# Optimization experiments

Hardware: AMD Instinct MI355X
Metric: run time of the kernel (lower is better)

Reference implementation:

```python
import jax, jax.numpy as jnp
import numpy as np

P_TOKENS = 200  # num_prompt_tokens
N_HEADS = 4


def setup_inputs() -> dict:
    key = jax.random.key(0)
    ks = jax.random.split(key, 6)
    B, N, C = 64, 1224, 1024
    D = 256  # bottleneck / down_size
    s = 0.02
    return {
        "x": jax.random.normal(ks[0], (B, N, C), dtype=jnp.float32),
        "down_W": jax.random.normal(ks[1], (D, C), dtype=jnp.float32) * s,
        "down_b": jnp.zeros((D,), jnp.float32),
        "up_W": jax.random.normal(ks[2], (C, D), dtype=jnp.float32) * s,
        "up_b": jnp.zeros((C,), jnp.float32),
        "in_proj_W": jax.random.normal(ks[3], (3 * D, D), dtype=jnp.float32) * s,
        "in_proj_b": jnp.zeros((3 * D,), jnp.float32),
        "out_proj_W": jax.random.normal(ks[4], (D, D), dtype=jnp.float32) * s,
        "out_proj_b": jnp.zeros((D,), jnp.float32),
        "gate": jnp.float32(1.0),
    }


def _forward(x, down_W, down_b, up_W, up_b, in_proj_W, in_proj_b,
             out_proj_W, out_proj_b, gate):
    B, N, C = x.shape
    E = down_W.shape[0]
    hd = E // N_HEADS
    # down projection + exact GELU (torch nn.GELU default)
    down = jax.nn.gelu(x @ down_W.T + down_b, approximate=False)  # [B,N,E]
    prompt = down[:, :P_TOKENS, :]   # [B,P,E]
    tok = down[:, P_TOKENS:, :]      # [B,T,E]
    # --- nn.MultiheadAttention(prompt, prompt, prompt) ---
    qkv = prompt @ in_proj_W.T + in_proj_b            # [B,P,3E]
    q, k, v = jnp.split(qkv, 3, axis=-1)
    def heads(t):
        return t.reshape(B, P_TOKENS, N_HEADS, hd)
    q, k, v = heads(q), heads(k), heads(v)
    attn = jnp.einsum('bqhd,bkhd->bhqk', q, k) / jnp.sqrt(jnp.float32(hd))
    attn = jax.nn.softmax(attn, axis=-1)
    sa = jnp.einsum('bhqk,bkhd->bqhd', attn, v).reshape(B, P_TOKENS, E)
    sa = sa @ out_proj_W.T + out_proj_b               # [B,P,E]
    # --- manual cross attention prompt -> tokens ---
    scale = jnp.float32(E) ** -0.5
    cross = jax.nn.softmax(jnp.einsum('bpe,bte->bpt', sa, tok) * scale, axis=-1)
    prompt_out = jnp.einsum('bpt,bte->bpe', cross, tok)  # [B,P,E]
    combined = jnp.concatenate([prompt_out, tok], axis=1)  # [B,N,E]
    up = combined @ up_W.T + up_b                          # [B,N,C]
    return gate * up


def reference(x, down_W, down_b, up_W, up_b, in_proj_W, in_proj_b,
              out_proj_W, out_proj_b, gate):
    return _forward(x, down_W, down_b, up_W, up_b, in_proj_W, in_proj_b,
                    out_proj_W, out_proj_b, gate)
```

## Files before the change

kernel.cpp:

```cpp
#include <hip/hip_runtime.h>
#include <math.h>

#define BB 64
#define NN 1224
#define CC 1024
#define DD 256
#define PP 200
#define TT 1024
#define HH 4
#define HDD 64

typedef __attribute__((ext_vector_type(8))) short bf16x8;
typedef __attribute__((ext_vector_type(4))) float f32x4;
typedef unsigned short u16;
typedef unsigned long long u64;

__device__ __forceinline__ u16 f2bf(float f) {
  union { float f; unsigned int u; } v; v.f = f;
  unsigned int r = v.u + 0x7FFF + ((v.u >> 16) & 1);
  return (u16)(r >> 16);
}
__device__ __forceinline__ float bf2f(u16 h) {
  union { unsigned int u; float f; } v; v.u = ((unsigned int)h) << 16;
  return v.f;
}
__device__ __forceinline__ unsigned int pk2(float a, float b) {
  return (unsigned int)f2bf(a) | ((unsigned int)f2bf(b) << 16);
}
__device__ __forceinline__ void gload16(const void* g, void* l) {
  __builtin_amdgcn_global_load_lds(
      (const __attribute__((address_space(1))) void*)g,
      (__attribute__((address_space(3))) void*)l, 16, 0, 0);
}
__device__ __forceinline__ f32x4 ntld4(const float* p) {
  return __builtin_nontemporal_load((const f32x4*)p);
}

static const size_t SZ_DOWN = (size_t)BB * NN * DD * 2;
static const size_t SZ_TOKT = (size_t)BB * DD * TT * 2;
static const size_t SZ_Q    = (size_t)BB * HH * PP * HDD * 2;
static const size_t SZ_SCORES = (size_t)BB * PP * TT * 2;

static const size_t B_DOWN   = 0;
static const size_t B_TOKT   = B_DOWN + SZ_DOWN;
static const size_t B_POOL   = B_TOKT + SZ_TOKT;
static const size_t B_QB     = B_POOL;
static const size_t B_KB     = B_QB + SZ_Q;
static const size_t B_VB     = B_KB + SZ_Q;
static const size_t B_SA     = B_VB + SZ_Q;
static const size_t B_SA2    = B_SA + SZ_Q;
static const size_t B_PBF    = B_POOL;
static const size_t B_POUTBF = B_SA2;
static const size_t B_SCORES = B_SA2 + SZ_Q;
static const size_t B_W      = B_SCORES + SZ_SCORES * 2;
static const size_t B_WD     = B_W;
static const size_t B_WU     = B_WD + 524288;
static const size_t B_WIP    = B_WU + 524288;
static const size_t B_WOP    = B_WIP + 393216;

#define MFMA_STEP64(Ab, Bb) \
  _Pragma("unroll") \
  for (int kk = 0; kk < 64; kk += 32) { \
    bf16x8 af[4], bfr[2]; \
    _Pragma("unroll") \
    for (int mi = 0; mi < 4; ++mi) { \
      const int R = mi * 16 + (lane & 15); \
      const int byt = (R * 128 + (kk + (lane >> 4) * 8) * 2) ^ ((R & 7) << 4); \
      af[mi] = *(const bf16x8*)((const char*)Ab + byt); \
    } \
    _Pragma("unroll") \
    for (int ni = 0; ni < 2; ++ni) { \
      const int R = wave * 32 + ni * 16 + (lane & 15); \
      const int byt = (R * 128 + (kk + (lane >> 4) * 8) * 2) ^ ((R & 7) << 4); \
      bfr[ni] = *(const bf16x8*)((const char*)Bb + byt); \
    } \
    _Pragma("unroll") \
    for (int mi = 0; mi < 4; ++mi) \
      _Pragma("unroll") \
      for (int ni = 0; ni < 2; ++ni) \
        acc[mi][ni] = __builtin_amdgcn_mfma_f32_16x16x32_bf16(af[mi], bfr[ni], acc[mi][ni], 0, 0, 0); \
  }

#define GLOAD_A1(Ab, SRC) \
  { \
    const int L = wave * 1024 + lane * 16; \
    const int r = L >> 7; \
    const int ce = ((L & 127) ^ ((r & 7) << 4)) >> 1; \
    gload16((SRC), (char*)Ab + wave * 1024); \
  }

#define GLOAD_B4(Bb, SRC) \
  _Pragma("unroll") \
  for (int ii = 0; ii < 4; ++ii) { \
    const int slot = wave * 4 + ii; \
    const int L = slot * 1024 + lane * 16; \
    const int r = L >> 7; \
    const int ce = ((L & 127) ^ ((r & 7) << 4)) >> 1; \
    gload16((SRC), (char*)Bb + slot * 1024); \
  }

#define PIPE_WAIT(N) asm volatile("s_waitcnt vmcnt(" #N ")" ::: "memory");
#define PIPE_BAR() \
  __builtin_amdgcn_s_barrier(); \
  __builtin_amdgcn_sched_barrier(0);
#define PIPE_END() \
  asm volatile("s_waitcnt lgkmcnt(0)" ::: "memory"); \
  __builtin_amdgcn_s_barrier(); \
  __builtin_amdgcn_sched_barrier(0);

__global__ __launch_bounds__(256) void k_castw(const float* __restrict__ dW,
                                               const float* __restrict__ uW,
                                               const float* __restrict__ iW,
                                               const float* __restrict__ oW,
                                               u16* __restrict__ dWb, u16* __restrict__ uWb,
                                               u16* __restrict__ iWb, u16* __restrict__ oWb)
{
  const int id = blockIdx.x * 256 + threadIdx.x;
  const float* s; u16* d; int off;
  if (id < 65536)       { s = dW; d = dWb; off = id; }
  else if (id < 131072) { s = uW; d = uWb; off = id - 65536; }
  else if (id < 180224) { s = iW; d = iWb; off = id - 131072; }
  else                  { s = oW; d = oWb; off = id - 180224; }
  const float4 v = ((const float4*)s)[off];
  uint2 p; p.x = pk2(v.x, v.y); p.y = pk2(v.z, v.w);
  *(uint2*)&d[(size_t)off * 4] = p;
}

__global__ __launch_bounds__(512) void k_down(const float* __restrict__ x,
                                              const u16* __restrict__ Wd,
                                              const float* __restrict__ bias,
                                              u16* __restrict__ out)
{
  __shared__ u16 Ab[2][64 * 64];
  __shared__ u16 Bb[2][256 * 64];
  const int tid = threadIdx.x;
  const int lane = tid & 63, wave = tid >> 6;
  f32x4 acc[4][2] = {};
  const int m0 = blockIdx.x * 64;
  const int ar0 = tid >> 4;
  const int c4 = (tid & 15) * 4;

  f32x4 areg[2];
#pragma unroll
  for (int i = 0; i < 2; ++i)
    areg[i] = ntld4(&x[(size_t)(m0 + ar0 + 32 * i) * CC + c4]);
#pragma unroll
  for (int i = 0; i < 2; ++i) {
    const int r = ar0 + 32 * i;
    uint2 p; p.x = pk2(areg[i].x, areg[i].y); p.y = pk2(areg[i].z, areg[i].w);
    *(uint2*)((char*)Ab[0] + ((r * 128 + c4 * 2) ^ ((r & 7) << 4))) = p;
  }
  GLOAD_B4(Bb[0], &Wd[(size_t)r * CC + 0 + ce])
#pragma unroll
  for (int i = 0; i < 2; ++i)
    areg[i] = ntld4(&x[(size_t)(m0 + ar0 + 32 * i) * CC + 64 + c4]);

  for (int it = 0; it < 16; ++it) {
    const int cur = it & 1;
    if (it < 14) {
#pragma unroll
      for (int i = 0; i < 2; ++i) {
        const int r = ar0 + 32 * i;
        uint2 p; p.x = pk2(areg[i].x, areg[i].y); p.y = pk2(areg[i].z, areg[i].w);
        *(uint2*)((char*)Ab[cur ^ 1] + ((r * 128 + c4 * 2) ^ ((r & 7) << 4))) = p;
      }
      const int kx = (it + 2) * 64;
#pragma unroll
      for (int i = 0; i < 2; ++i)
        areg[i] = ntld4(&x[(size_t)(m0 + ar0 + 32 * i) * CC + kx + c4]);
      const int kb = (it + 1) * 64;
      GLOAD_B4(Bb[cur ^ 1], &Wd[(size_t)r * CC + kb + ce])
      asm volatile("s_waitcnt vmcnt(6) lgkmcnt(0)" ::: "memory");
    } else if (it == 14) {
#pragma unroll
      for (int i = 0; i < 2; ++i) {
        const int r = ar0 + 32 * i;
        uint2 p; p.x = pk2(areg[i].x, areg[i].y); p.y = pk2(areg[i].z, areg[i].w);
        *(uint2*)((char*)Ab[cur ^ 1] + ((r * 128 + c4 * 2) ^ ((r & 7) << 4))) = p;
      }
      GLOAD_B4(Bb[cur ^ 1], &Wd[(size_t)r * CC + 960 + ce])
      asm volatile("s_waitcnt vmcnt(4) lgkmcnt(0)" ::: "memory");
    } else {
      asm volatile("s_waitcnt vmcnt(0) lgkmcnt(0)" ::: "memory");
    }
    PIPE_BAR()
    MFMA_STEP64(Ab[cur], Bb[cur])
    PIPE_END()
  }
#pragma unroll
  for (int mi = 0; mi < 4; ++mi) {
#pragma unroll
    for (int ni = 0; ni < 2; ++ni) {
      const int col = wave * 32 + ni * 16 + (lane & 15);
      const float bv = bias[col];
#pragma unroll
      for (int r = 0; r < 4; ++r) {
        const int row = m0 + mi * 16 + (lane >> 4) * 4 + r;
        float v = acc[mi][ni][r] + bv;
        v = 0.5f * v * (1.f + erff(v * 0.7071067811865475f));
        out[(size_t)row * DD + col] = f2bf(v);
      }
    }
  }
}

__global__ __launch_bounds__(256) void k_tokT(const u16* __restrict__ down,
                                              u16* __restrict__ tokT)
{
  __shared__ u16 Ls[64][68];
  const int b = blockIdx.z;
  const int t0 = blockIdx.x * 64, e0 = blockIdx.y * 64;
  const int tid = threadIdx.x;
#pragma unroll
  for (int it = 0; it < 4; ++it) {
    const int idx = tid + 256 * it;
    const int r = idx >> 4, c4 = (idx & 15) * 4;
    const u64 v = *(const u64*)&down[((size_t)(b * NN + PP + t0 + r)) * DD + e0 + c4];
    *(u64*)&Ls[r][c4] = v;
  }
  __syncthreads();
#pragma unroll
  for (int it = 0; it < 4; ++it) {
    const int idx = tid + 256 * it;
    const int re = idx >> 4, c4 = (idx & 15) * 4;
    u64 pk = (u64)Ls[c4 + 0][re] | ((u64)Ls[c4 + 1][re] << 16) |
             ((u64)Ls[c4 + 2][re] << 32) | ((u64)Ls[c4 + 3][re] << 48);
    *(u64*)&tokT[((size_t)(b * DD + e0 + re)) * TT + t0 + c4] = pk;
  }
}

__global__ __launch_bounds__(512) void k_qkv(const u16* __restrict__ down,
                                             const u16* __restrict__ Wip,
                                             const float* __restrict__ bias,
                                             u16* __restrict__ qb,
                                             u16* __restrict__ kb,
                                             u16* __restrict__ vb)
{
  __shared__ u16 Ab[2][64 * 64];
  __shared__ u16 Bb[2][256 * 64];
  const int tid = threadIdx.x;
  const int lane = tid & 63, wave = tid >> 6;
  f32x4 acc[4][2] = {};
  const int m0 = blockIdx.x * 64;
  const int nt = blockIdx.y;

#define QKV_A(BUF, K0) GLOAD_A1(BUF, ({ const int m = m0 + r; const int b = m / PP; const int p = m - b * PP; \
                    &down[((size_t)(b * NN + p)) * DD + (K0) + ce]; }))
  QKV_A(Ab[0], 0)
  GLOAD_B4(Bb[0], &Wip[(size_t)(nt * 256 + r) * DD + 0 + ce])
  for (int it = 0; it < 4; ++it) {
    const int cur = it & 1;
    if (it < 3) {
      const int k0 = (it + 1) * 64;
      QKV_A(Ab[cur ^ 1], k0)
      GLOAD_B4(Bb[cur ^ 1], &Wip[(size_t)(nt * 256 + r) * DD + k0 + ce])
      PIPE_WAIT(5)
    } else { PIPE_WAIT(0) }
    PIPE_BAR()
    MFMA_STEP64(Ab[cur], Bb[cur])
    PIPE_END()
  }
#undef QKV_A
  u16* dst = (nt == 0) ? qb : ((nt == 1) ? kb : vb);
#pragma unroll
  for (int mi = 0; mi < 4; ++mi) {
#pragma unroll
    for (int ni = 0; ni < 2; ++ni) {
      const int n = wave * 32 + ni * 16 + (lane & 15);
      const float bv = bias[nt * 256 + n];
      const int h = n >> 6, dd = n & 63;
#pragma unroll
      for (int r = 0; r < 4; ++r) {
        const int m = m0 + mi * 16 + (lane >> 4) * 4 + r;
        const int b = m / PP, p = m - b * PP;
        dst[(((size_t)(b * HH + h)) * PP + p) * HDD + dd] = f2bf(acc[mi][ni][r] + bv);
      }
    }
  }
}

__global__ __launch_bounds__(256) void k_attn(const u16* __restrict__ qb,
                                              const u16* __restrict__ kb,
                                              const u16* __restrict__ vb,
                                              u16* __restrict__ sa)
{
  __shared__ u16 Ks[208 * 64];
  __shared__ u16 Vt[64 * 232];
  __shared__ u16 Pb[4 * 16 * 232];
  const int tid = threadIdx.x, lane = tid & 63, wave = tid >> 6;
  const int bh = blockIdx.x;
  const size_t kvbase = (size_t)bh * (PP * HDD);

  for (int it = 0; it < 13; ++it) {
    const int idx = tid + 256 * it;
    if (idx < 3200) {
      const int e = idx * 4;
      const int j = e >> 6, d = e & 63;
      const u64 kv = *(const u64*)&kb[kvbase + e];
      const int byt = (j * 128 + d * 2) ^ ((j & 7) << 4);
      *(u64*)((char*)Ks + byt) = kv;
      const u64 vv = *(const u64*)&vb[kvbase + e];
      const u16* vp = (const u16*)&vv;
#pragma unroll
      for (int w = 0; w < 4; ++w) Vt[(d + w) * 232 + j] = vp[w];
    }
  }
  if (tid < 128) {
    const int rr = 200 + (tid >> 4), c = (tid & 15) * 4;
    const int byt = (rr * 128 + c * 2) ^ ((rr & 7) << 4);
    *(u64*)((char*)Ks + byt) = 0ULL;
  }
#pragma unroll
  for (int w = 0; w < 2; ++w) {
    const int idx = tid + 256 * w;
    const int d = idx >> 3, cg = idx & 7;
    *(u64*)&Vt[d * 232 + 200 + cg * 4] = 0ULL;
  }
  {
    u16* pw = Pb + wave * (16 * 232);
#pragma unroll
    for (int w = 0; w < 2; ++w) {
      const int idx = lane + 64 * w;
      if (idx < 96) {
        const int row = idx / 6, cg = idx - row * 6;
        *(u64*)&pw[row * 232 + 208 + cg * 4] = 0ULL;
      }
    }
  }
  __syncthreads();

  const int b_ = bh >> 2, h = bh & 3;
  const u16* qbase = qb + kvbase;
  u16* pw = Pb + wave * (16 * 232);

  for (int f = wave; f < 13; f += 4) {
    int qrow = f * 16 + (lane & 15); if (qrow > 199) qrow = 199;
    bf16x8 qa[2];
#pragma unroll
    for (int kk = 0; kk < 2; ++kk)
      qa[kk] = *(const bf16x8*)&qbase[(size_t)qrow * 64 + kk * 32 + (lane >> 4) * 8];

    f32x4 s[13];
#pragma unroll
    for (int nf = 0; nf < 13; ++nf) {
      const int R = nf * 16 + (lane & 15);
      f32x4 a = {};
#pragma unroll
      for (int kk = 0; kk < 2; ++kk) {
        const int byt = (R * 128 + (kk * 32 + (lane >> 4) * 8) * 2) ^ ((R & 7) << 4);
        const bf16x8 kf = *(const bf16x8*)((const char*)Ks + byt);
        a = __builtin_amdgcn_mfma_f32_16x16x32_bf16(qa[kk], kf, a, 0, 0, 0);
      }
      s[nf] = a;
    }
    float mx[4] = {-1e30f, -1e30f, -1e30f, -1e30f};
#pragma unroll
    for (int nf = 0; nf < 13; ++nf) {
      const int col = nf * 16 + (lane & 15);
#pragma unroll
      for (int r = 0; r < 4; ++r) {
        float v = (col < PP) ? s[nf][r] * 0.125f : -INFINITY;
        s[nf][r] = v;
        mx[r] = fmaxf(mx[r], v);
      }
    }
#pragma unroll
    for (int off = 1; off < 16; off <<= 1)
#pragma unroll
      for (int r = 0; r < 4; ++r) mx[r] = fmaxf(mx[r], __shfl_xor(mx[r], off));
    float sum[4] = {0.f, 0.f, 0.f, 0.f};
#pragma unroll
    for (int nf = 0; nf < 13; ++nf)
#pragma unroll
      for (int r = 0; r < 4; ++r) {
        const float e = expf(s[nf][r] - mx[r]);
        s[nf][r] = e;
        sum[r] += e;
      }
#pragma unroll
    for (int off = 1; off < 16; off <<= 1)
#pragma unroll
      for (int r = 0; r < 4; ++r) sum[r] += __shfl_xor(sum[r], off);
    float inv[4];
#pragma unroll
    for (int r = 0; r < 4; ++r) inv[r] = 1.f / sum[r];
#pragma unroll
    for (int nf = 0; nf < 13; ++nf) {
      const int col = nf * 16 + (lane & 15);
#pragma unroll
      for (int r = 0; r < 4; ++r) {
        const int row = (lane >> 4) * 4 + r;
        pw[row * 232 + col] = f2bf(s[nf][r] * inv[r]);
      }
    }
    f32x4 o[4] = {};
#pragma unroll
    for (int kk = 0; kk < 7; ++kk) {
      const bf16x8 pa = *(const bf16x8*)((const char*)pw +
                         ((lane & 15) * 232 + kk * 32 + (lane >> 4) * 8) * 2);
#pragma unroll
      for (int nf4 = 0; nf4 < 4; ++nf4) {
        const bf16x8 vv = *(const bf16x8*)((const char*)Vt +
                           (((lane & 15) + 16 * nf4) * 232 + kk * 32 + (lane >> 4) * 8) * 2);
        o[nf4] = __builtin_amdgcn_mfma_f32_16x16x32_bf16(pa, vv, o[nf4], 0, 0, 0);
      }
    }
#pragma unroll
    for (int nf4 = 0; nf4 < 4; ++nf4) {
      const int d = (lane & 15) + 16 * nf4;
#pragma unroll
      for (int r = 0; r < 4; ++r) {
        const int p = f * 16 + (lane >> 4) * 4 + r;
        if (p < PP)
          sa[((size_t)(b_ * PP + p)) * DD + h * HDD + d] = f2bf(o[nf4][r]);
      }
    }
  }
}

__global__ __launch_bounds__(512) void k_oproj(const u16* __restrict__ A,
                                               const u16* __restrict__ Wop,
                                               const float* __restrict__ bias,
                                               u16* __restrict__ out)
{
  __shared__ u16 Ab[2][64 * 64];
  __shared__ u16 Bb[2][256 * 64];
  const int tid = threadIdx.x;
  const int lane = tid & 63, wave = tid >> 6;
  f32x4 acc[4][2] = {};
  const int m0 = blockIdx.x * 64;

  GLOAD_A1(Ab[0], &A[(size_t)(m0 + r) * DD + 0 + ce])
  GLOAD_B4(Bb[0], &Wop[(size_t)r * DD + 0 + ce])
  for (int it = 0; it < 4; ++it) {
    const int cur = it & 1;
    if (it < 3) {
      const int k0 = (it + 1) * 64;
      GLOAD_A1(Ab[cur ^ 1], &A[(size_t)(m0 + r) * DD + k0 + ce])
      GLOAD_B4(Bb[cur ^ 1], &Wop[(size_t)r * DD + k0 + ce])
      PIPE_WAIT(5)
    } else { PIPE_WAIT(0) }
    PIPE_BAR()
    MFMA_STEP64(Ab[cur], Bb[cur])
    PIPE_END()
  }
#pragma unroll
  for (int mi = 0; mi < 4; ++mi) {
#pragma unroll
    for (int ni = 0; ni < 2; ++ni) {
      const int col = wave * 32 + ni * 16 + (lane & 15);
      const float bv = bias[col];
#pragma unroll
      for (int r = 0; r < 4; ++r) {
        const int row = m0 + mi * 16 + (lane >> 4) * 4 + r;
        out[(size_t)row * DD + col] = f2bf(acc[mi][ni][r] + bv);
      }
    }
  }
}

__global__ __launch_bounds__(512) void k_scores(const u16* __restrict__ sa2,
                                                const u16* __restrict__ down,
                                                u16* __restrict__ scores)
{
  __shared__ u16 Ab[2][64 * 64];
  __shared__ u16 Bb[2][256 * 64];
  const int tid = threadIdx.x;
  const int lane = tid & 63, wave = tid >> 6;
  f32x4 acc[4][2] = {};
  const int b = blockIdx.x, mh = blockIdx.y, nt = blockIdx.z;

#define SC_A(BUF, K0) GLOAD_A1(BUF, ({ int p = mh * 64 + r; p = (p < PP) ? p : (PP - 1); \
                    &sa2[((size_t)(b * PP + p)) * DD + (K0) + ce]; }))
  SC_A(Ab[0], 0)
  GLOAD_B4(Bb[0], &down[((size_t)(b * NN + PP + nt * 256 + r)) * DD + 0 + ce])
  for (int it = 0; it < 4; ++it) {
    const int cur = it & 1;
    if (it < 3) {
      const int k0 = (it + 1) * 64;
      SC_A(Ab[cur ^ 1], k0)
      GLOAD_B4(Bb[cur ^ 1], &down[((size_t)(b * NN + PP + nt * 256 + r)) * DD + k0 + ce])
      PIPE_WAIT(5)
    } else { PIPE_WAIT(0) }
    PIPE_BAR()
    MFMA_STEP64(Ab[cur], Bb[cur])
    PIPE_END()
  }
#undef SC_A
#pragma unroll
  for (int mi = 0; mi < 4; ++mi) {
#pragma unroll
    for (int ni = 0; ni < 2; ++ni) {
      const int t = nt * 256 + wave * 32 + ni * 16 + (lane & 15);
#pragma unroll
      for (int r = 0; r < 4; ++r) {
        const int p = mh * 64 + mi * 16 + (lane >> 4) * 4 + r;
        if (p < PP)
          scores[((size_t)(b * PP + p)) * TT + t] = f2bf(acc[mi][ni][r] * 0.0625f);
      }
    }
  }
}

__global__ __launch_bounds__(256) void k_softmax(const u16* __restrict__ s,
                                                 u16* __restrict__ pbf)
{
  const int row = blockIdx.x;
  const int t = threadIdx.x;
  const int lane = t & 63, w = t >> 6;
  __shared__ float red[4];
  const u64 raw = *(const u64*)&s[(size_t)row * TT + t * 4];
  float v[4];
#pragma unroll
  for (int i = 0; i < 4; ++i) v[i] = bf2f((u16)(raw >> (16 * i)));
  float mx = fmaxf(fmaxf(v[0], v[1]), fmaxf(v[2], v[3]));
#pragma unroll
  for (int off = 32; off; off >>= 1) mx = fmaxf(mx, __shfl_xor(mx, off));
  if (lane == 0) red[w] = mx;
  __syncthreads();
  mx = fmaxf(fmaxf(red[0], red[1]), fmaxf(red[2], red[3]));
  __syncthreads();
  float sum = 0.f;
#pragma unroll
  for (int i = 0; i < 4; ++i) { v[i] = expf(v[i] - mx); sum += v[i]; }
#pragma unroll
  for (int off = 32; off; off >>= 1) sum += __shfl_xor(sum, off);
  if (lane == 0) red[w] = sum;
  __syncthreads();
  sum = red[0] + red[1] + red[2] + red[3];
  const float inv = 1.f / sum;
  u64 pk = (u64)f2bf(v[0] * inv) | ((u64)f2bf(v[1] * inv) << 16) |
           ((u64)f2bf(v[2] * inv) << 32) | ((u64)f2bf(v[3] * inv) << 48);
  *(u64*)&pbf[(size_t)row * TT + t * 4] = pk;
}

__global__ __launch_bounds__(512) void k_pout(const u16* __restrict__ pbf,
                                              const u16* __restrict__ tokT,
                                              u16* __restrict__ out)
{
  __shared__ u16 Ab[2][64 * 64];
  __shared__ u16 Bb[2][256 * 64];
  const int tid = threadIdx.x;
  const int lane = tid & 63, wave = tid >> 6;
  f32x4 acc[4][2] = {};
  const int b = blockIdx.x, mh = blockIdx.y;

#define PO_A(BUF, K0) GLOAD_A1(BUF, ({ int p = mh * 64 + r; p = (p < PP) ? p : (PP - 1); \
                    &pbf[((size_t)(b * PP + p)) * TT + (K0) + ce]; }))
  PO_A(Ab[0], 0)
  GLOAD_B4(Bb[0], &tokT[((size_t)(b * DD + r)) * TT + 0 + ce])
  for (int it = 0; it < 16; ++it) {
    const int cur = it & 1;
    if (it < 15) {
      const int k0 = (it + 1) * 64;
      PO_A(Ab[cur ^ 1], k0)
      GLOAD_B4(Bb[cur ^ 1], &tokT[((size_t)(b * DD + r)) * TT + k0 + ce])
      PIPE_WAIT(5)
    } else { PIPE_WAIT(0) }
    PIPE_BAR()
    MFMA_STEP64(Ab[cur], Bb[cur])
    PIPE_END()
  }
#undef PO_A
#pragma unroll
  for (int mi = 0; mi < 4; ++mi) {
#pragma unroll
    for (int ni = 0; ni < 2; ++ni) {
      const int e = wave * 32 + ni * 16 + (lane & 15);
#pragma unroll
      for (int r = 0; r < 4; ++r) {
        const int p = mh * 64 + mi * 16 + (lane >> 4) * 4 + r;
        if (p < PP)
          out[((size_t)(b * PP + p)) * DD + e] = f2bf(acc[mi][ni][r]);
      }
    }
  }
}

__global__ __launch_bounds__(512) void k_up(const u16* __restrict__ poutbf,
                                            const u16* __restrict__ down,
                                            const u16* __restrict__ Wu,
                                            const float* __restrict__ bias,
                                            const float* __restrict__ gate,
                                            float* __restrict__ out)
{
  __shared__ u16 Ab[2][64 * 64];
  __shared__ u16 Bb[2][256 * 64];
  const int tid = threadIdx.x;
  const int lane = tid & 63, wave = tid >> 6;
  f32x4 acc[4][2] = {};
  const int m0 = blockIdx.x * 64;
  const int n0 = blockIdx.y * 256;

#define UP_A(BUF, K0) GLOAD_A1(BUF, ({ const int m = m0 + r; const int b = m / NN; const int rr = m - b * NN; \
                     const u16* base = (rr < PP) ? &poutbf[((size_t)(b * PP + rr)) * DD] \
                                                 : &down[((size_t)(b * NN + rr)) * DD]; \
                     base + (K0) + ce; }))
  UP_A(Ab[0], 0)
  GLOAD_B4(Bb[0], &Wu[(size_t)(n0 + r) * DD + 0 + ce])
  for (int it = 0; it < 4; ++it) {
    const int cur = it & 1;
    if (it < 3) {
      const int k0 = (it + 1) * 64;
      UP_A(Ab[cur ^ 1], k0)
      GLOAD_B4(Bb[cur ^ 1], &Wu[(size_t)(n0 + r) * DD + k0 + ce])
      PIPE_WAIT(5)
    } else { PIPE_WAIT(0) }
    PIPE_BAR()
    MFMA_STEP64(Ab[cur], Bb[cur])
    PIPE_END()
  }
#undef UP_A
  const float g = gate[0];
#pragma unroll
  for (int mi = 0; mi < 4; ++mi) {
#pragma unroll
    for (int ni = 0; ni < 2; ++ni) {
      const int col = n0 + wave * 32 + ni * 16 + (lane & 15);
      const float bv = bias[col];
#pragma unroll
      for (int r = 0; r < 4; ++r) {
        const int row = m0 + mi * 16 + (lane >> 4) * 4 + r;
        __builtin_nontemporal_store((acc[mi][ni][r] + bv) * g, &out[(size_t)row * CC + col]);
      }
    }
  }
}

extern "C" void kernel_launch(void* const* d_in, const int* in_sizes, int n_in,
                              void* d_out, int out_size, void* d_ws, size_t ws_size,
                              hipStream_t stream) {
  const float* x          = (const float*)d_in[0];
  const float* down_W     = (const float*)d_in[1];
  const float* down_b     = (const float*)d_in[2];
  const float* up_W       = (const float*)d_in[3];
  const float* up_b       = (const float*)d_in[4];
  const float* in_proj_W  = (const float*)d_in[5];
  const float* in_proj_b  = (const float*)d_in[6];
  const float* out_proj_W = (const float*)d_in[7];
  const float* out_proj_b = (const float*)d_in[8];
  const float* gate       = (const float*)d_in[9];
  float* out = (float*)d_out;

  char* wsb = (char*)d_ws;
  u16* down_bf = (u16*)(wsb + B_DOWN);
  u16* tokT    = (u16*)(wsb + B_TOKT);
  u16* qb      = (u16*)(wsb + B_QB);
  u16* kb      = (u16*)(wsb + B_KB);
  u16* vb      = (u16*)(wsb + B_VB);
  u16* sa_bf   = (u16*)(wsb + B_SA);
  u16* sa2_bf  = (u16*)(wsb + B_SA2);
  u16* pbf     = (u16*)(wsb + B_PBF);
  u16* poutbf  = (u16*)(wsb + B_POUTBF);
  u16* scores  = (u16*)(wsb + B_SCORES);
  u16* Wd  = (u16*)(wsb + B_WD);
  u16* Wu  = (u16*)(wsb + B_WU);
  u16* Wip = (u16*)(wsb + B_WIP);
  u16* Wop = (u16*)(wsb + B_WOP);

  k_castw<<<dim3(768), 256, 0, stream>>>(down_W, up_W, in_proj_W, out_proj_W, Wd, Wu, Wip, Wop);
  k_down<<<dim3((BB * NN) / 64), 512, 0, stream>>>(x, Wd, down_b, down_bf);
  k_tokT<<<dim3(16, 4, BB), 256, 0, stream>>>(down_bf, tokT);
  k_qkv<<<dim3(200, 3), 512, 0, stream>>>(down_bf, Wip, in_proj_b, qb, kb, vb);
  k_attn<<<dim3(BB * HH), 256, 0, stream>>>(qb, kb, vb, sa_bf);
  k_oproj<<<dim3(200), 512, 0, stream>>>(sa_bf, Wop, out_proj_b, sa2_bf);
  k_scores<<<dim3(BB, 4, 4), 512, 0, stream>>>(sa2_bf, down_bf, scores);
  k_softmax<<<dim3(BB * PP), 256, 0, stream>>>(scores, pbf);
  k_pout<<<dim3(BB, 4), 512, 0, stream>>>(pbf, tokT, poutbf);
  k_up<<<dim3((BB * NN) / 64, CC / 256), 512, 0, stream>>>(poutbf, down_bf, Wu, up_b, gate, out);
}
```

Baseline: 317.6 us.

## Fuse token transpose into down-projection epilogue and widen attention blocks

The down-projection epilogue now also writes the transposed token activations directly, so the separate transpose kernel and its extra read and write of the bottleneck tensor are removed. The self-attention kernel moves from 4 to 8 waves per block so each wave handles fewer query tiles. In exchange, the transposed writes from the GEMM epilogue are strided 8-byte stores that coalesce less well, and attention uses more shared memory per block.

```diff
diff --git a/kernel.cpp b/kernel.cpp
--- a/kernel.cpp
+++ b/kernel.cpp
@@ -129,7 +129,8 @@
 __global__ __launch_bounds__(512) void k_down(const float* __restrict__ x,
                                               const u16* __restrict__ Wd,
                                               const float* __restrict__ bias,
-                                              u16* __restrict__ out)
+                                              u16* __restrict__ out,
+                                              u16* __restrict__ tokT)
 {
   __shared__ u16 Ab[2][64 * 64];
   __shared__ u16 Bb[2][256 * 64];
@@ -193,39 +194,22 @@
     for (int ni = 0; ni < 2; ++ni) {
       const int col = wave * 32 + ni * 16 + (lane & 15);
       const float bv = bias[col];
+      u16 vs[4];
 #pragma unroll
       for (int r = 0; r < 4; ++r) {
         const int row = m0 + mi * 16 + (lane >> 4) * 4 + r;
         float v = acc[mi][ni][r] + bv;
         v = 0.5f * v * (1.f + erff(v * 0.7071067811865475f));
-        out[(size_t)row * DD + col] = f2bf(v);
-      }
-    }
-  }
-}
-
-__global__ __launch_bounds__(256) void k_tokT(const u16* __restrict__ down,
-                                              u16* __restrict__ tokT)
-{
-  __shared__ u16 Ls[64][68];
-  const int b = blockIdx.z;
-  const int t0 = blockIdx.x * 64, e0 = blockIdx.y * 64;
-  const int tid = threadIdx.x;
-#pragma unroll
-  for (int it = 0; it < 4; ++it) {
-    const int idx = tid + 256 * it;
-    const int r = idx >> 4, c4 = (idx & 15) * 4;
-    const u64 v = *(const u64*)&down[((size_t)(b * NN + PP + t0 + r)) * DD + e0 + c4];
-    *(u64*)&Ls[r][c4] = v;
-  }
-  __syncthreads();
-#pragma unroll
-  for (int it = 0; it < 4; ++it) {
-    const int idx = tid + 256 * it;
-    const int re = idx >> 4, c4 = (idx & 15) * 4;
-    u64 pk = (u64)Ls[c4 + 0][re] | ((u64)Ls[c4 + 1][re] << 16) |
-             ((u64)Ls[c4 + 2][re] << 32) | ((u64)Ls[c4 + 3][re] << 48);
-    *(u64*)&tokT[((size_t)(b * DD + e0 + re)) * TT + t0 + c4] = pk;
+        vs[r] = f2bf(v);
+        out[(size_t)row * DD + col] = vs[r];
+      }
+      const int row0 = m0 + mi * 16 + (lane >> 4) * 4;
+      const int b = row0 / NN, rr = row0 - b * NN;
+      if (rr >= PP) {
+        const u64 pk = (u64)vs[0] | ((u64)vs[1] << 16) | ((u64)vs[2] << 32) | ((u64)vs[3] << 48);
+        *(u64*)&tokT[((size_t)(b * DD + col)) * TT + (rr - PP)] = pk;
+      }
+    }
   }
 }
 
@@ -279,20 +263,20 @@
   }
 }
 
-__global__ __launch_bounds__(256) void k_attn(const u16* __restrict__ qb,
+__global__ __launch_bounds__(512) void k_attn(const u16* __restrict__ qb,
                                               const u16* __restrict__ kb,
                                               const u16* __restrict__ vb,
                                               u16* __restrict__ sa)
 {
   __shared__ u16 Ks[208 * 64];
   __shared__ u16 Vt[64 * 232];
-  __shared__ u16 Pb[4 * 16 * 232];
+  __shared__ u16 Pb[8 * 16 * 232];
   const int tid = threadIdx.x, lane = tid & 63, wave = tid >> 6;
   const int bh = blockIdx.x;
   const size_t kvbase = (size_t)bh * (PP * HDD);
 
-  for (int it = 0; it < 13; ++it) {
-    const int idx = tid + 256 * it;
+  for (int it = 0; it < 7; ++it) {
+    const int idx = tid + 512 * it;
     if (idx < 3200) {
       const int e = idx * 4;
       const int j = e >> 6, d = e & 63;
@@ -310,10 +294,8 @@
     const int byt = (rr * 128 + c * 2) ^ ((rr & 7) << 4);
     *(u64*)((char*)Ks + byt) = 0ULL;
   }
-#pragma unroll
-  for (int w = 0; w < 2; ++w) {
-    const int idx = tid + 256 * w;
-    const int d = idx >> 3, cg = idx & 7;
+  {
+    const int d = tid >> 3, cg = tid & 7;
     *(u64*)&Vt[d * 232 + 200 + cg * 4] = 0ULL;
   }
   {
@@ -333,7 +315,7 @@
   const u16* qbase = qb + kvbase;
   u16* pw = Pb + wave * (16 * 232);
 
-  for (int f = wave; f < 13; f += 4) {
+  for (int f = wave; f < 13; f += 8) {
     int qrow = f * 16 + (lane & 15); if (qrow > 199) qrow = 199;
     bf16x8 qa[2];
 #pragma unroll
@@ -659,10 +641,9 @@
   u16* Wop = (u16*)(wsb + B_WOP);
 
   k_castw<<<dim3(768), 256, 0, stream>>>(down_W, up_W, in_proj_W, out_proj_W, Wd, Wu, Wip, Wop);
-  k_down<<<dim3((BB * NN) / 64), 512, 0, stream>>>(x, Wd, down_b, down_bf);
-  k_tokT<<<dim3(16, 4, BB), 256, 0, stream>>>(down_bf, tokT);
+  k_down<<<dim3((BB * NN) / 64), 512, 0, stream>>>(x, Wd, down_b, down_bf, tokT);
   k_qkv<<<dim3(200, 3), 512, 0, stream>>>(down_bf, Wip, in_proj_b, qb, kb, vb);
-  k_attn<<<dim3(BB * HH), 256, 0, stream>>>(qb, kb, vb, sa_bf);
+  k_attn<<<dim3(BB * HH), 512, 0, stream>>>(qb, kb, vb, sa_bf);
   k_oproj<<<dim3(200), 512, 0, stream>>>(sa_bf, Wop, out_proj_b, sa2_bf);
   k_scores<<<dim3(BB, 4, 4), 512, 0, stream>>>(sa2_bf, down_bf, scores);
   k_softmax<<<dim3(BB * PP), 256, 0, stream>>>(scores, pbf);
```

After: 309.7 us. -2.5%, faster.
